# Kernel tuning notes

Measured on AMD Instinct MI355X. Metric: run time of the kernel, lower is better.

The kernel has to match this reference:

```python
import jax, jax.numpy as jnp
import numpy as np

N_FRAME = 8
FOLD_DIV = 3

def setup_inputs() -> dict:
    key = jax.random.key(0)
    x = jax.random.normal(key, (128, 96, 56, 56), dtype=jnp.float32)  # (B*T, C, H, W)
    return {"x": x}

def reference(x) -> jnp.ndarray:
    bt, c, h, w = x.shape
    fold = c // FOLD_DIV
    # (B, T, C, H, W)
    x5 = x.reshape(-1, N_FRAME, c, h, w)
    g1 = x5[:, :, :fold]           # shift toward past: frame t gets t+1, last frame zero
    g2 = x5[:, :, fold:2 * fold]   # shift toward future: frame t gets t-1, first frame zero
    g3 = x5[:, :, 2 * fold:]       # unchanged
    out1 = jnp.concatenate([g1[:, 1:], jnp.zeros_like(g1[:, :1])], axis=1)
    out2 = jnp.concatenate([jnp.zeros_like(g2[:, :1]), g2[:, :-1]], axis=1)
    out = jnp.concatenate([out1, out2, g3], axis=2)
    return out.reshape(bt, c, h, w)
```

## Files before the change

kernel.cpp:

```cpp
#include <hip/hip_runtime.h>


#define C_TOT   96
#define FOLD    32
#define NFRAME  8
#define HW4     784
#define NPLANES 12288

typedef float v4f __attribute__((ext_vector_type(4)));

__global__ __launch_bounds__(256) void tsm_kernel(const v4f* __restrict__ in,
                                                  v4f* __restrict__ out) {
    const int plane = blockIdx.x;
    const int c = plane % C_TOT;
    const int t = (plane / C_TOT) % NFRAME;

    int  delta = 0;
    bool zero  = false;
    if (c < FOLD)          { delta =  C_TOT; zero = (t == NFRAME - 1); }
    else if (c < 2 * FOLD) { delta = -C_TOT; zero = (t == 0); }

    const long base = (long)plane * HW4;
    v4f* o = out + base;
    const int j = threadIdx.x;

    if (zero) {
        const v4f z = (v4f){0.f, 0.f, 0.f, 0.f};
        __builtin_nontemporal_store(z, &o[j]);
        __builtin_nontemporal_store(z, &o[j + 256]);
        __builtin_nontemporal_store(z, &o[j + 512]);
        if (j < HW4 - 768) __builtin_nontemporal_store(z, &o[j + 768]);
    } else {
        const v4f* s = in + base + (long)delta * HW4;
        v4f a0 = __builtin_nontemporal_load(&s[j]);
        v4f a1 = __builtin_nontemporal_load(&s[j + 256]);
        v4f a2 = __builtin_nontemporal_load(&s[j + 512]);
        v4f a3;
        const bool tail = (j < HW4 - 768);
        if (tail) a3 = __builtin_nontemporal_load(&s[j + 768]);
        __builtin_nontemporal_store(a0, &o[j]);
        __builtin_nontemporal_store(a1, &o[j + 256]);
        __builtin_nontemporal_store(a2, &o[j + 512]);
        if (tail) __builtin_nontemporal_store(a3, &o[j + 768]);
    }
}

extern "C" void kernel_launch(void* const* d_in, const int* in_sizes, int n_in,
                              void* d_out, int out_size, void* d_ws, size_t ws_size,
                              hipStream_t stream) {
    const v4f* x   = (const v4f*)d_in[0];
    v4f*       out = (v4f*)d_out;
    tsm_kernel<<<NPLANES, 256, 0, stream>>>(x, out);
}
```

Baseline: 246.1 us.

## Process 16 contiguous channel planes per block with a 7-deep unrolled copy loop

Each block now handles a chunk of 16 contiguous planes, which is 12544 float4s, and launches 768 blocks instead of 12288. The whole chunk shares one shift/zero decision because 16 divides the fold of 32. Each thread runs 49 iterations that batch 7 loads before 7 nontemporal stores, so more reads are in flight and the per-plane tail branch goes away. Source loads switch from nontemporal to normal loads. With 768 blocks of 256 threads the GPU may be under-occupied, which could hurt memory-level parallelism on a device with 256 CUs.

Result: slower. 267.5 us (+8.7%).

```diff
diff --git a/kernel.cpp b/kernel.cpp
--- a/kernel.cpp
+++ b/kernel.cpp
@@ -5,43 +5,50 @@
 #define FOLD    32
 #define NFRAME  8
 #define HW4     784
-#define NPLANES 12288
+#define CHUNK   16
+#define NCHUNKS 768
+#define ITERS   49
 
 typedef float v4f __attribute__((ext_vector_type(4)));
 
 __global__ __launch_bounds__(256) void tsm_kernel(const v4f* __restrict__ in,
                                                   v4f* __restrict__ out) {
-    const int plane = blockIdx.x;
-    const int c = plane % C_TOT;
-    const int t = (plane / C_TOT) % NFRAME;
+    const int plane0 = blockIdx.x * CHUNK;
+    const int c0 = plane0 % C_TOT;
+    const int t  = (plane0 / C_TOT) % NFRAME;
 
     int  delta = 0;
     bool zero  = false;
-    if (c < FOLD)          { delta =  C_TOT; zero = (t == NFRAME - 1); }
-    else if (c < 2 * FOLD) { delta = -C_TOT; zero = (t == 0); }
+    if (c0 < FOLD)          { delta =  C_TOT; zero = (t == NFRAME - 1); }
+    else if (c0 < 2 * FOLD) { delta = -C_TOT; zero = (t == 0); }
 
-    const long base = (long)plane * HW4;
-    v4f* o = out + base;
-    const int j = threadIdx.x;
+    const long base = (long)plane0 * HW4;
+    v4f* __restrict__ o = out + base + threadIdx.x;
 
     if (zero) {
         const v4f z = (v4f){0.f, 0.f, 0.f, 0.f};
-        __builtin_nontemporal_store(z, &o[j]);
-        __builtin_nontemporal_store(z, &o[j + 256]);
-        __builtin_nontemporal_store(z, &o[j + 512]);
-        if (j < HW4 - 768) __builtin_nontemporal_store(z, &o[j + 768]);
+        #pragma unroll 7
+        for (int k = 0; k < ITERS; ++k)
+            __builtin_nontemporal_store(z, &o[k * 256]);
     } else {
-        const v4f* s = in + base + (long)delta * HW4;
-        v4f a0 = __builtin_nontemporal_load(&s[j]);
-        v4f a1 = __builtin_nontemporal_load(&s[j + 256]);
-        v4f a2 = __builtin_nontemporal_load(&s[j + 512]);
-        v4f a3;
-        const bool tail = (j < HW4 - 768);
-        if (tail) a3 = __builtin_nontemporal_load(&s[j + 768]);
-        __builtin_nontemporal_store(a0, &o[j]);
-        __builtin_nontemporal_store(a1, &o[j + 256]);
-        __builtin_nontemporal_store(a2, &o[j + 512]);
-        if (tail) __builtin_nontemporal_store(a3, &o[j + 768]);
+        const v4f* __restrict__ s = in + base + (long)delta * HW4 + threadIdx.x;
+        #pragma unroll 1
+        for (int k = 0; k < ITERS; k += 7) {
+            const v4f a0 = s[(k + 0) * 256];
+            const v4f a1 = s[(k + 1) * 256];
+            const v4f a2 = s[(k + 2) * 256];
+            const v4f a3 = s[(k + 3) * 256];
+            const v4f a4 = s[(k + 4) * 256];
+            const v4f a5 = s[(k + 5) * 256];
+            const v4f a6 = s[(k + 6) * 256];
+            __builtin_nontemporal_store(a0, &o[(k + 0) * 256]);
+            __builtin_nontemporal_store(a1, &o[(k + 1) * 256]);
+            __builtin_nontemporal_store(a2, &o[(k + 2) * 256]);
+            __builtin_nontemporal_store(a3, &o[(k + 3) * 256]);
+            __builtin_nontemporal_store(a4, &o[(k + 4) * 256]);
+            __builtin_nontemporal_store(a5, &o[(k + 5) * 256]);
+            __builtin_nontemporal_store(a6, &o[(k + 6) * 256]);
+        }
     }
 }
 
@@ -50,5 +57,5 @@
                               hipStream_t stream) {
     const v4f* x   = (const v4f*)d_in[0];
     v4f*       out = (v4f*)d_out;
-    tsm_kernel<<<NPLANES, 256, 0, stream>>>(x, out);
+    tsm_kernel<<<NCHUNKS, 256, 0, stream>>>(x, out);
 }
```
